# Performance work log

Measured on AMD Instinct MI355X. Metric: run time of the kernel, lower is better.

The kernel has to match this reference:

```python
import jax, jax.numpy as jnp
import numpy as np

N_CODES = 1024
DIM = 64
COMMITMENT = 0.25


def setup_inputs() -> dict:
    key = jax.random.key(0)
    k1, k2 = jax.random.split(key)
    z = jax.random.normal(k1, (32, DIM, 64, 64), dtype=jnp.float32)
    # nn.Embedding weight initialized uniform(-1/n_codes, 1/n_codes)
    codebook = jax.random.uniform(
        k2, (N_CODES, DIM), dtype=jnp.float32,
        minval=-1.0 / N_CODES, maxval=1.0 / N_CODES)
    return {"z": z, "codebook": codebook}


def reference(z, codebook):
    B, C, H, W = z.shape
    # (B,C,H,W) -> (B*H*W, C)
    z_flat = jnp.transpose(z, (0, 2, 3, 1)).reshape(-1, C)
    # squared L2 distances via expansion: |z|^2 + |e|^2 - 2 z.e
    dists = (
        jnp.sum(z_flat ** 2, axis=1, keepdims=True)
        + jnp.sum(codebook ** 2, axis=1)
        - 2.0 * z_flat @ codebook.T
    )  # [N, n_codes]
    indices = jnp.argmin(dists, axis=1)  # [N]
    z_q = jnp.transpose(codebook[indices].reshape(B, H, W, C), (0, 3, 1, 2))
    commit_loss = jnp.mean((jax.lax.stop_gradient(z_q) - z) ** 2)
    codebook_loss = jnp.mean((z_q - jax.lax.stop_gradient(z)) ** 2)
    vq_loss = codebook_loss + COMMITMENT * commit_loss
    z_q_st = z + jax.lax.stop_gradient(z_q - z)  # straight-through
    return (z_q_st, vq_loss)
```

## Files before the change

kernel.cpp:

```cpp
#include <hip/hip_runtime.h>


constexpr int DIM    = 64;
constexpr int NCODES = 1024;
constexpr int HWSZ   = 4096;
constexpr int NPOS   = 131072;
constexpr int BLOCK  = 256;
constexpr int PPB    = 128;
constexpr int GRID   = NPOS / PPB;

typedef float    f32x4  __attribute__((ext_vector_type(4)));
typedef float    f32x2  __attribute__((ext_vector_type(2)));
typedef unsigned uint2v __attribute__((ext_vector_type(2)));
typedef unsigned uint4v __attribute__((ext_vector_type(4)));

__global__ __launch_bounds__(256) void vq_prep(const float* __restrict__ cb,
                                               float* __restrict__ cinitT,
                                               unsigned* __restrict__ cbq) {
    int j = blockIdx.x * 256 + threadIdx.x;
    const float4* src = (const float4*)(cb + (size_t)j * DIM);
    unsigned words[16];
    float nq = 0.f;
#pragma unroll
    for (int g8 = 0; g8 < 8; g8++) {
        float4 v0 = src[g8 * 2], v1 = src[g8 * 2 + 1];
        int lo = 0, hi = 0;
        lo = __builtin_amdgcn_cvt_pk_fp8_f32(v0.x * 512.f, v0.y * 512.f, lo, 0);
        lo = __builtin_amdgcn_cvt_pk_fp8_f32(v0.z * 512.f, v0.w * 512.f, lo, 1);
        hi = __builtin_amdgcn_cvt_pk_fp8_f32(v1.x * 512.f, v1.y * 512.f, hi, 0);
        hi = __builtin_amdgcn_cvt_pk_fp8_f32(v1.z * 512.f, v1.w * 512.f, hi, 1);
        words[g8 * 2] = (unsigned)lo; words[g8 * 2 + 1] = (unsigned)hi;
#pragma unroll
        for (int m = 0; m < 2; m++) {
            int wv = m ? hi : lo;
            f32x2 d0 = __builtin_amdgcn_cvt_pk_f32_fp8(wv, 0);
            f32x2 d1 = __builtin_amdgcn_cvt_pk_f32_fp8(wv, 1);
            nq += d0[0] * d0[0] + d0[1] * d0[1] + d1[0] * d1[0] + d1[1] * d1[1];
        }
    }
#pragma unroll
    for (int u = 0; u < 4; u++) {
        uint4v t = {words[2 * u], words[2 * u + 1],
                    words[2 * u + 8], words[2 * u + 9]};
        *(uint4v*)(cbq + (size_t)j * 16 + u * 4) = t;
    }
    cinitT[(j & 15) * 64 + (j >> 4)] = 8.f - nq * (1.f / 1024.f);
}

__global__ __launch_bounds__(BLOCK, 4) void vq_main(const float* __restrict__ z,
                                                    const float* __restrict__ cinitT,
                                                    const unsigned char* __restrict__ cbq,
                                                    float* __restrict__ out) {
    __shared__ int   bj_lds[PPB];
    __shared__ float ls_lds[BLOCK / 64];

    const int tid  = threadIdx.x;
    const int w    = tid >> 6;
    const int lane = tid & 63;
    const int q    = lane >> 4;
    const int r    = lane & 15;
    const int p0   = blockIdx.x * PPB;
    const int b    = p0 >> 12;
    const int hwb  = p0 & 4095;

    long  afrag[2][2];
    float zsq[2];
#pragma unroll
    for (int s = 0; s < 2; s++) {
        const float* zb = z + (size_t)b * DIM * HWSZ + hwb + w * 32 + s * 16 + r;
        float sq = 0.f;
#pragma unroll
        for (int h = 0; h < 2; h++) {
            float v[8];
#pragma unroll
            for (int i = 0; i < 8; i++) {
                v[i] = zb[(size_t)(h * 32 + q * 8 + i) * HWSZ];
                sq = fmaf(v[i], v[i], sq);
            }
            int lo = 0, hi = 0;
            lo = __builtin_amdgcn_cvt_pk_fp8_f32(v[0], v[1], lo, 0);
            lo = __builtin_amdgcn_cvt_pk_fp8_f32(v[2], v[3], lo, 1);
            hi = __builtin_amdgcn_cvt_pk_fp8_f32(v[4], v[5], hi, 0);
            hi = __builtin_amdgcn_cvt_pk_fp8_f32(v[6], v[7], hi, 1);
            uint2v u = {(unsigned)lo, (unsigned)hi};
            afrag[s][h] = __builtin_bit_cast(long, u);
        }
        sq += __shfl_xor(sq, 16, 64);
        sq += __shfl_xor(sq, 32, 64);
        zsq[s] = sq;
    }

    const int bbase = r * 64 + q * 16;
    const float* cip = cinitT + r * 64;

    const unsigned char* bp0 = cbq + 0 * 1024 + bbase;
    const unsigned char* bp1 = cbq + 1 * 1024 + bbase;
    const unsigned char* bp2 = cbq + 2 * 1024 + bbase;
    const unsigned char* bp3 = cbq + 3 * 1024 + bbase;

    uint4v Bp[4];
    Bp[0] = *(const uint4v*)bp0;  bp0 += 4096;
    Bp[1] = *(const uint4v*)bp1;  bp1 += 4096;
    Bp[2] = *(const uint4v*)bp2;  bp2 += 4096;
    Bp[3] = *(const uint4v*)bp3;  bp3 += 4096;
    float4 ci[2];
    ci[0] = *(const float4*)(cip + 0);
    ci[1] = *(const float4*)(cip + 4);

    float best0[4], best1[4], tmp0[4], tmp1[4];
#pragma unroll
    for (int g = 0; g < 4; g++) { best0[g] = 0.f; best1[g] = 0.f; }

    f32x4 accR[3][2];

    auto ISSUE = [&](int jt) {
        const int slot = jt & 3;
        const float cin = ci[(jt >> 2) & 1][jt & 3];
        uint2v blo = {Bp[slot][0], Bp[slot][1]};
        uint2v bhi = {Bp[slot][2], Bp[slot][3]};
        f32x4 c0 = {cin, cin, cin, cin};
        f32x4 a0 = __builtin_amdgcn_mfma_f32_16x16x32_fp8_fp8(
            afrag[0][0], __builtin_bit_cast(long, blo), c0, 0, 0, 0);
        a0 = __builtin_amdgcn_mfma_f32_16x16x32_fp8_fp8(
            afrag[0][1], __builtin_bit_cast(long, bhi), a0, 0, 0, 0);
        f32x4 a1 = __builtin_amdgcn_mfma_f32_16x16x32_fp8_fp8(
            afrag[1][0], __builtin_bit_cast(long, blo), c0, 0, 0, 0);
        a1 = __builtin_amdgcn_mfma_f32_16x16x32_fp8_fp8(
            afrag[1][1], __builtin_bit_cast(long, bhi), a1, 0, 0, 0);
        accR[jt % 3][0] = a0;
        accR[jt % 3][1] = a1;
        if (slot == 0)      { Bp[0] = *(const uint4v*)bp0;  bp0 += 4096; }
        else if (slot == 1) { Bp[1] = *(const uint4v*)bp1;  bp1 += 4096; }
        else if (slot == 2) { Bp[2] = *(const uint4v*)bp2;  bp2 += 4096; }
        else                { Bp[3] = *(const uint4v*)bp3;  bp3 += 4096; }
        if ((jt & 3) == 3)
            ci[(jt >> 2) & 1] =
                *(const float4*)(cip + ((((jt >> 2) + 2) & 15) * 4));
    };

    auto PROCESS = [&](int pj) {
        const unsigned tag = (unsigned)(1023 - pj * 16) - (unsigned)r;
#pragma unroll
        for (int g = 0; g < 4; g++) {
            unsigned bits0 = (__float_as_uint(accR[pj % 3][0][g]) & ~1023u)
                           | (tag & 1023u);
            unsigned bits1 = (__float_as_uint(accR[pj % 3][1][g]) & ~1023u)
                           | (tag & 1023u);
            float pf0 = __uint_as_float(bits0);
            float pf1 = __uint_as_float(bits1);
            if ((pj & 1) == 0) {
                tmp0[g] = pf0; tmp1[g] = pf1;
            } else {
                best0[g] = fmaxf(fmaxf(best0[g], tmp0[g]), pf0);
                best1[g] = fmaxf(fmaxf(best1[g], tmp1[g]), pf1);
            }
        }
    };

    ISSUE(0);
    ISSUE(1);
#pragma unroll
    for (int jt = 2; jt < 64; jt++) {
        ISSUE(jt);
        PROCESS(jt - 2);
    }
    PROCESS(62);
    PROCESS(63);

    unsigned bestu0[4], bestu1[4];
#pragma unroll
    for (int g = 0; g < 4; g++) {
        unsigned v0 = __float_as_uint(best0[g]);
        unsigned v1 = __float_as_uint(best1[g]);
#pragma unroll
        for (int off = 1; off < 16; off <<= 1) {
            unsigned w0 = __shfl_xor((int)v0, off, 64);
            unsigned w1 = __shfl_xor((int)v1, off, 64);
            v0 = v0 > w0 ? v0 : w0;
            v1 = v1 > w1 ? v1 : w1;
        }
        bestu0[g] = v0; bestu1[g] = v1;
    }

    float lsum = 0.f;
    if (q == (r >> 2)) {
        int g = r & 3;
        unsigned v0 = bestu0[0], v1 = bestu1[0];
        v0 = (g == 1) ? bestu0[1] : v0;  v1 = (g == 1) ? bestu1[1] : v1;
        v0 = (g == 2) ? bestu0[2] : v0;  v1 = (g == 2) ? bestu1[2] : v1;
        v0 = (g == 3) ? bestu0[3] : v0;  v1 = (g == 3) ? bestu1[3] : v1;
        bj_lds[w * 32 + r]      = 1023 - (int)(v0 & 1023u);
        bj_lds[w * 32 + 16 + r] = 1023 - (int)(v1 & 1023u);
        lsum = zsq[0] + (8.f - __uint_as_float(v0)) * (1.f / 256.f)
             + zsq[1] + (8.f - __uint_as_float(v1)) * (1.f / 256.f);
    }
#pragma unroll
    for (int off = 32; off > 0; off >>= 1) lsum += __shfl_down(lsum, off, 64);
    if (lane == 0) ls_lds[w] = lsum;
    __syncthreads();
    if (tid == 0) {
        float s = ls_lds[0] + ls_lds[1] + ls_lds[2] + ls_lds[3];
        atomicAdd(out + (size_t)NPOS * DIM, s * (1.25f / 8388608.f));
    }

    int posi = tid & 127;
    int uu   = tid >> 7;
    int myj  = bj_lds[posi];
    float* ob = out + (size_t)b * DIM * HWSZ + hwb + posi;
#pragma unroll
    for (int k = 0; k < 2; k++) {
        int u  = uu + 2 * k;
        uint4v t = *(const uint4v*)(cbq + (size_t)myj * 64 + u * 16);
#pragma unroll
        for (int m = 0; m < 2; m++) {
            int cbase = (m == 0) ? (8 * u) : (32 + 8 * u);
#pragma unroll
            for (int wd = 0; wd < 2; wd++) {
                int word = (int)t[m * 2 + wd];
                f32x2 d0 = __builtin_amdgcn_cvt_pk_f32_fp8(word, 0);
                f32x2 d1 = __builtin_amdgcn_cvt_pk_f32_fp8(word, 1);
                ob[(size_t)(cbase + wd * 4 + 0) * HWSZ] = d0[0] * (1.f / 512.f);
                ob[(size_t)(cbase + wd * 4 + 1) * HWSZ] = d0[1] * (1.f / 512.f);
                ob[(size_t)(cbase + wd * 4 + 2) * HWSZ] = d1[0] * (1.f / 512.f);
                ob[(size_t)(cbase + wd * 4 + 3) * HWSZ] = d1[1] * (1.f / 512.f);
            }
        }
    }
}

extern "C" void kernel_launch(void* const* d_in, const int* in_sizes, int n_in,
                              void* d_out, int out_size, void* d_ws, size_t ws_size,
                              hipStream_t stream) {
    const float* z  = (const float*)d_in[0];
    const float* cb = (const float*)d_in[1];
    float* out = (float*)d_out;

    float*    cinitT = (float*)d_ws;
    unsigned* cbq    = (unsigned*)((char*)d_ws + 4096);

    hipMemsetAsync(out + (size_t)NPOS * DIM, 0, sizeof(float), stream);
    vq_prep<<<NCODES / 256, 256, 0, stream>>>(cb, cinitT, cbq);
    vq_main<<<GRID, BLOCK, 0, stream>>>(z, cinitT,
                                        (const unsigned char*)cbq, out);
}
```

Measured before the change: 116.7 us.

## Halve positions per block to one 16-row tile per wave, raising occupancy

Each wave now handles 16 positions instead of 32, so the block covers 64 positions and the grid doubles. Only one A fragment and one accumulator set are kept, and launch bounds now request 8 waves-per-EU occupancy instead of 4. This is meant to cut register pressure and improve latency hiding across memory and MFMA. The cost is that each codebook fragment loaded from global/L2 is reused by half as many MFMAs, which doubles codebook traffic per position and adds more blocks and atomics.

```diff
diff --git a/kernel.cpp b/kernel.cpp
--- a/kernel.cpp
+++ b/kernel.cpp
@@ -6,7 +6,7 @@
 constexpr int HWSZ   = 4096;
 constexpr int NPOS   = 131072;
 constexpr int BLOCK  = 256;
-constexpr int PPB    = 128;
+constexpr int PPB    = 64;
 constexpr int GRID   = NPOS / PPB;
 
 typedef float    f32x4  __attribute__((ext_vector_type(4)));
@@ -47,7 +47,7 @@
     cinitT[(j & 15) * 64 + (j >> 4)] = 8.f - nq * (1.f / 1024.f);
 }
 
-__global__ __launch_bounds__(BLOCK, 4) void vq_main(const float* __restrict__ z,
+__global__ __launch_bounds__(BLOCK, 8) void vq_main(const float* __restrict__ z,
                                                     const float* __restrict__ cinitT,
                                                     const unsigned char* __restrict__ cbq,
                                                     float* __restrict__ out) {
@@ -63,11 +63,10 @@
     const int b    = p0 >> 12;
     const int hwb  = p0 & 4095;
 
-    long  afrag[2][2];
-    float zsq[2];
-#pragma unroll
-    for (int s = 0; s < 2; s++) {
-        const float* zb = z + (size_t)b * DIM * HWSZ + hwb + w * 32 + s * 16 + r;
+    long  afrag[2];
+    float zsq;
+    {
+        const float* zb = z + (size_t)b * DIM * HWSZ + hwb + w * 16 + r;
         float sq = 0.f;
 #pragma unroll
         for (int h = 0; h < 2; h++) {
@@ -83,11 +82,11 @@
             hi = __builtin_amdgcn_cvt_pk_fp8_f32(v[4], v[5], hi, 0);
             hi = __builtin_amdgcn_cvt_pk_fp8_f32(v[6], v[7], hi, 1);
             uint2v u = {(unsigned)lo, (unsigned)hi};
-            afrag[s][h] = __builtin_bit_cast(long, u);
+            afrag[h] = __builtin_bit_cast(long, u);
         }
         sq += __shfl_xor(sq, 16, 64);
         sq += __shfl_xor(sq, 32, 64);
-        zsq[s] = sq;
+        zsq = sq;
     }
 
     const int bbase = r * 64 + q * 16;
@@ -107,11 +106,8 @@
     ci[0] = *(const float4*)(cip + 0);
     ci[1] = *(const float4*)(cip + 4);
 
-    float best0[4], best1[4], tmp0[4], tmp1[4];
-#pragma unroll
-    for (int g = 0; g < 4; g++) { best0[g] = 0.f; best1[g] = 0.f; }
-
-    f32x4 accR[3][2];
+    float best[4] = {0.f, 0.f, 0.f, 0.f};
+    f32x4 accR[3];
 
     auto ISSUE = [&](int jt) {
         const int slot = jt & 3;
@@ -120,15 +116,10 @@
         uint2v bhi = {Bp[slot][2], Bp[slot][3]};
         f32x4 c0 = {cin, cin, cin, cin};
         f32x4 a0 = __builtin_amdgcn_mfma_f32_16x16x32_fp8_fp8(
-            afrag[0][0], __builtin_bit_cast(long, blo), c0, 0, 0, 0);
+            afrag[0], __builtin_bit_cast(long, blo), c0, 0, 0, 0);
         a0 = __builtin_amdgcn_mfma_f32_16x16x32_fp8_fp8(
-            afrag[0][1], __builtin_bit_cast(long, bhi), a0, 0, 0, 0);
-        f32x4 a1 = __builtin_amdgcn_mfma_f32_16x16x32_fp8_fp8(
-            afrag[1][0], __builtin_bit_cast(long, blo), c0, 0, 0, 0);
-        a1 = __builtin_amdgcn_mfma_f32_16x16x32_fp8_fp8(
-            afrag[1][1], __builtin_bit_cast(long, bhi), a1, 0, 0, 0);
-        accR[jt % 3][0] = a0;
-        accR[jt % 3][1] = a1;
+            afrag[1], __builtin_bit_cast(long, bhi), a0, 0, 0, 0);
+        accR[jt % 3] = a0;
         if (slot == 0)      { Bp[0] = *(const uint4v*)bp0;  bp0 += 4096; }
         else if (slot == 1) { Bp[1] = *(const uint4v*)bp1;  bp1 += 4096; }
         else if (slot == 2) { Bp[2] = *(const uint4v*)bp2;  bp2 += 4096; }
@@ -142,18 +133,9 @@
         const unsigned tag = (unsigned)(1023 - pj * 16) - (unsigned)r;
 #pragma unroll
         for (int g = 0; g < 4; g++) {
-            unsigned bits0 = (__float_as_uint(accR[pj % 3][0][g]) & ~1023u)
-                           | (tag & 1023u);
-            unsigned bits1 = (__float_as_uint(accR[pj % 3][1][g]) & ~1023u)
-                           | (tag & 1023u);
-            float pf0 = __uint_as_float(bits0);
-            float pf1 = __uint_as_float(bits1);
-            if ((pj & 1) == 0) {
-                tmp0[g] = pf0; tmp1[g] = pf1;
-            } else {
-                best0[g] = fmaxf(fmaxf(best0[g], tmp0[g]), pf0);
-                best1[g] = fmaxf(fmaxf(best1[g], tmp1[g]), pf1);
-            }
+            unsigned bits = (__float_as_uint(accR[pj % 3][g]) & ~1023u)
+                          | (tag & 1023u);
+            best[g] = fmaxf(best[g], __uint_as_float(bits));
         }
     };
 
@@ -167,32 +149,27 @@
     PROCESS(62);
     PROCESS(63);
 
-    unsigned bestu0[4], bestu1[4];
+    unsigned bestu[4];
 #pragma unroll
     for (int g = 0; g < 4; g++) {
-        unsigned v0 = __float_as_uint(best0[g]);
-        unsigned v1 = __float_as_uint(best1[g]);
+        unsigned v = __float_as_uint(best[g]);
 #pragma unroll
         for (int off = 1; off < 16; off <<= 1) {
-            unsigned w0 = __shfl_xor((int)v0, off, 64);
-            unsigned w1 = __shfl_xor((int)v1, off, 64);
-            v0 = v0 > w0 ? v0 : w0;
-            v1 = v1 > w1 ? v1 : w1;
-        }
-        bestu0[g] = v0; bestu1[g] = v1;
+            unsigned v2 = __shfl_xor((int)v, off, 64);
+            v = v > v2 ? v : v2;
+        }
+        bestu[g] = v;
     }
 
     float lsum = 0.f;
     if (q == (r >> 2)) {
         int g = r & 3;
-        unsigned v0 = bestu0[0], v1 = bestu1[0];
-        v0 = (g == 1) ? bestu0[1] : v0;  v1 = (g == 1) ? bestu1[1] : v1;
-        v0 = (g == 2) ? bestu0[2] : v0;  v1 = (g == 2) ? bestu1[2] : v1;
-        v0 = (g == 3) ? bestu0[3] : v0;  v1 = (g == 3) ? bestu1[3] : v1;
-        bj_lds[w * 32 + r]      = 1023 - (int)(v0 & 1023u);
-        bj_lds[w * 32 + 16 + r] = 1023 - (int)(v1 & 1023u);
-        lsum = zsq[0] + (8.f - __uint_as_float(v0)) * (1.f / 256.f)
-             + zsq[1] + (8.f - __uint_as_float(v1)) * (1.f / 256.f);
+        unsigned v = bestu[0];
+        v = (g == 1) ? bestu[1] : v;
+        v = (g == 2) ? bestu[2] : v;
+        v = (g == 3) ? bestu[3] : v;
+        bj_lds[w * 16 + r] = 1023 - (int)(v & 1023u);
+        lsum = zsq + (8.f - __uint_as_float(v)) * (1.f / 256.f);
     }
 #pragma unroll
     for (int off = 32; off > 0; off >>= 1) lsum += __shfl_down(lsum, off, 64);
@@ -203,27 +180,23 @@
         atomicAdd(out + (size_t)NPOS * DIM, s * (1.25f / 8388608.f));
     }
 
-    int posi = tid & 127;
-    int uu   = tid >> 7;
+    int posi = tid & 63;
+    int u    = tid >> 6;
     int myj  = bj_lds[posi];
+    uint4v t = *(const uint4v*)(cbq + (size_t)myj * 64 + u * 16);
     float* ob = out + (size_t)b * DIM * HWSZ + hwb + posi;
 #pragma unroll
-    for (int k = 0; k < 2; k++) {
-        int u  = uu + 2 * k;
-        uint4v t = *(const uint4v*)(cbq + (size_t)myj * 64 + u * 16);
-#pragma unroll
-        for (int m = 0; m < 2; m++) {
-            int cbase = (m == 0) ? (8 * u) : (32 + 8 * u);
-#pragma unroll
-            for (int wd = 0; wd < 2; wd++) {
-                int word = (int)t[m * 2 + wd];
-                f32x2 d0 = __builtin_amdgcn_cvt_pk_f32_fp8(word, 0);
-                f32x2 d1 = __builtin_amdgcn_cvt_pk_f32_fp8(word, 1);
-                ob[(size_t)(cbase + wd * 4 + 0) * HWSZ] = d0[0] * (1.f / 512.f);
-                ob[(size_t)(cbase + wd * 4 + 1) * HWSZ] = d0[1] * (1.f / 512.f);
-                ob[(size_t)(cbase + wd * 4 + 2) * HWSZ] = d1[0] * (1.f / 512.f);
-                ob[(size_t)(cbase + wd * 4 + 3) * HWSZ] = d1[1] * (1.f / 512.f);
-            }
+    for (int m = 0; m < 2; m++) {
+        int cbase = (m == 0) ? (8 * u) : (32 + 8 * u);
+#pragma unroll
+        for (int wd = 0; wd < 2; wd++) {
+            int word = (int)t[m * 2 + wd];
+            f32x2 d0 = __builtin_amdgcn_cvt_pk_f32_fp8(word, 0);
+            f32x2 d1 = __builtin_amdgcn_cvt_pk_f32_fp8(word, 1);
+            ob[(size_t)(cbase + wd * 4 + 0) * HWSZ] = d0[0] * (1.f / 512.f);
+            ob[(size_t)(cbase + wd * 4 + 1) * HWSZ] = d0[1] * (1.f / 512.f);
+            ob[(size_t)(cbase + wd * 4 + 2) * HWSZ] = d1[0] * (1.f / 512.f);
+            ob[(size_t)(cbase + wd * 4 + 3) * HWSZ] = d1[1] * (1.f / 512.f);
         }
     }
 }
```

Measured after the change: 157.4 us. +34.9%, slower.

## Split codebook gather into separate epilogue kernel with vectorized float4 stores

Applied to the files above, without the earlier changes.

The argmin sweep now writes the selected code indices to a workspace buffer instead of gathering and storing z_q itself. A new epilogue kernel has each thread handle four consecutive positions, so it can emit 16-byte float4 stores along the spatial dimension in place of scalar strided stores. This is meant to improve write coalescing for the 32 MB output and to keep the store-heavy phase out of the compute-bound sweep kernel. The cost is an extra launch and a small round trip of the indices through global memory.

```diff
diff --git a/kernel.cpp b/kernel.cpp
--- a/kernel.cpp
+++ b/kernel.cpp
@@ -47,10 +47,11 @@
     cinitT[(j & 15) * 64 + (j >> 4)] = 8.f - nq * (1.f / 1024.f);
 }
 
-__global__ __launch_bounds__(BLOCK, 4) void vq_main(const float* __restrict__ z,
-                                                    const float* __restrict__ cinitT,
-                                                    const unsigned char* __restrict__ cbq,
-                                                    float* __restrict__ out) {
+__global__ __launch_bounds__(BLOCK, 4) void vq_sweep(const float* __restrict__ z,
+                                                     const float* __restrict__ cinitT,
+                                                     const unsigned char* __restrict__ cbq,
+                                                     int* __restrict__ bjg,
+                                                     float* __restrict__ out) {
     __shared__ int   bj_lds[PPB];
     __shared__ float ls_lds[BLOCK / 64];
 
@@ -203,27 +204,50 @@
         atomicAdd(out + (size_t)NPOS * DIM, s * (1.25f / 8388608.f));
     }
 
-    int posi = tid & 127;
-    int uu   = tid >> 7;
-    int myj  = bj_lds[posi];
-    float* ob = out + (size_t)b * DIM * HWSZ + hwb + posi;
-#pragma unroll
-    for (int k = 0; k < 2; k++) {
-        int u  = uu + 2 * k;
-        uint4v t = *(const uint4v*)(cbq + (size_t)myj * 64 + u * 16);
-#pragma unroll
-        for (int m = 0; m < 2; m++) {
-            int cbase = (m == 0) ? (8 * u) : (32 + 8 * u);
+    if (tid < PPB) bjg[p0 + tid] = bj_lds[tid];
+}
+
+__global__ __launch_bounds__(256, 8) void vq_epi(const int* __restrict__ bjg,
+                                                 const unsigned char* __restrict__ cbq,
+                                                 float* __restrict__ out) {
+    const int tid = threadIdx.x;
+    const int pq  = tid & 63;
+    const int u2  = tid >> 6;
+    const int p0  = blockIdx.x * 256;
+    const int b   = p0 >> 12;
+    const int hwb = p0 & 4095;
+
+    int4 bj4 = *(const int4*)(bjg + p0 + 4 * pq);
+
+    uint4v t0 = *(const uint4v*)(cbq + (size_t)bj4.x * 64 + u2 * 16);
+    uint4v t1 = *(const uint4v*)(cbq + (size_t)bj4.y * 64 + u2 * 16);
+    uint4v t2 = *(const uint4v*)(cbq + (size_t)bj4.z * 64 + u2 * 16);
+    uint4v t3 = *(const uint4v*)(cbq + (size_t)bj4.w * 64 + u2 * 16);
+
+    float* ob = out + (size_t)b * DIM * HWSZ + hwb + 4 * pq;
+#pragma unroll
+    for (int m = 0; m < 2; m++) {
+        int cbase = (m == 0) ? (8 * u2) : (32 + 8 * u2);
+        float vals[4][8];
+#pragma unroll
+        for (int k = 0; k < 4; k++) {
+            uint4v tk = (k == 0) ? t0 : (k == 1) ? t1 : (k == 2) ? t2 : t3;
 #pragma unroll
             for (int wd = 0; wd < 2; wd++) {
-                int word = (int)t[m * 2 + wd];
+                int word = (int)tk[m * 2 + wd];
                 f32x2 d0 = __builtin_amdgcn_cvt_pk_f32_fp8(word, 0);
                 f32x2 d1 = __builtin_amdgcn_cvt_pk_f32_fp8(word, 1);
-                ob[(size_t)(cbase + wd * 4 + 0) * HWSZ] = d0[0] * (1.f / 512.f);
-                ob[(size_t)(cbase + wd * 4 + 1) * HWSZ] = d0[1] * (1.f / 512.f);
-                ob[(size_t)(cbase + wd * 4 + 2) * HWSZ] = d1[0] * (1.f / 512.f);
-                ob[(size_t)(cbase + wd * 4 + 3) * HWSZ] = d1[1] * (1.f / 512.f);
+                vals[k][wd * 4 + 0] = d0[0];
+                vals[k][wd * 4 + 1] = d0[1];
+                vals[k][wd * 4 + 2] = d1[0];
+                vals[k][wd * 4 + 3] = d1[1];
             }
+        }
+#pragma unroll
+        for (int c = 0; c < 8; c++) {
+            f32x4 fv = {vals[0][c] * (1.f / 512.f), vals[1][c] * (1.f / 512.f),
+                        vals[2][c] * (1.f / 512.f), vals[3][c] * (1.f / 512.f)};
+            *(f32x4*)(ob + (size_t)(cbase + c) * HWSZ) = fv;
         }
     }
 }
@@ -237,9 +261,11 @@
 
     float*    cinitT = (float*)d_ws;
     unsigned* cbq    = (unsigned*)((char*)d_ws + 4096);
+    int*      bjg    = (int*)((char*)d_ws + 4096 + 73728);
 
     hipMemsetAsync(out + (size_t)NPOS * DIM, 0, sizeof(float), stream);
     vq_prep<<<NCODES / 256, 256, 0, stream>>>(cb, cinitT, cbq);
-    vq_main<<<GRID, BLOCK, 0, stream>>>(z, cinitT,
-                                        (const unsigned char*)cbq, out);
-}
+    vq_sweep<<<GRID, BLOCK, 0, stream>>>(z, cinitT,
+                                         (const unsigned char*)cbq, bjg, out);
+    vq_epi<<<NPOS / 256, 256, 0, stream>>>(bjg, (const unsigned char*)cbq, out);
+}
```

Result: slower. 124.6 us (+6.7%).
